# Kernel optimization log

Measured on AMD Instinct MI355X. Metric: run time of the kernel, lower is better.

Reference implementation:

```python
import jax, jax.numpy as jnp
import numpy as np

B, T, J, D = 32, 1024, 256, 512

def setup_inputs() -> dict:
    key = jax.random.key(0)
    k1, k2, k3 = jax.random.split(key, 3)
    h = jax.random.normal(k1, (B, T, D), dtype=jnp.float32)
    u = jax.random.normal(k2, (B, J, D), dtype=jnp.float32)
    w = jax.random.normal(k3, (1, 3 * D), dtype=jnp.float32) * 0.05
    return {"h": h, "u": u, "w": w}

def reference(h, u, w):
    # S[b,i,j] = w . concat([h_i, u_j, h_i*u_j])
    # Algebraic decomposition: w = [w_h, w_u, w_m]
    d = h.shape[-1]
    w = w[0]
    w_h, w_u, w_m = w[:d], w[d:2*d], w[2*d:]
    # [B,T,1] + [B,1,J] + [B,T,J]
    term_h = jnp.einsum('btd,d->bt', h, w_h)[:, :, None]
    term_u = jnp.einsum('bjd,d->bj', u, w_u)[:, None, :]
    term_m = jnp.einsum('btd,bjd->btj', h * w_m, u)
    return term_h + term_u + term_m
```

## Files before the change

### kernel.cpp

```cpp
#include <hip/hip_runtime.h>
#include <hip/hip_bf16.h>
#include <stdint.h>

#define B_ 32
#define T_ 1024
#define J_ 256
#define D_ 512

typedef __attribute__((ext_vector_type(8))) short short8;
typedef __attribute__((ext_vector_type(4))) float floatx4;

__global__ __launch_bounds__(256) void prep_u_kernel(
    const float* __restrict__ u, const float* __restrict__ w,
    __hip_bfloat16* __restrict__ B2, float* __restrict__ tu)
{
    int row  = blockIdx.x * 4 + (threadIdx.x >> 6);
    int lane = threadIdx.x & 63;
    const float* src = u + (size_t)row * D_;
    int base = lane * 8;

    float4 v0  = *(const float4*)(src + base);
    float4 v1  = *(const float4*)(src + base + 4);
    float4 wh0 = *(const float4*)(w + base);
    float4 wh1 = *(const float4*)(w + base + 4);
    float4 wu0 = *(const float4*)(w + D_ + base);
    float4 wu1 = *(const float4*)(w + D_ + base + 4);
    float4 wm0 = *(const float4*)(w + 2*D_ + base);
    float4 wm1 = *(const float4*)(w + 2*D_ + base + 4);

    float s = v0.x*wu0.x + v0.y*wu0.y + v0.z*wu0.z + v0.w*wu0.w
            + v1.x*wu1.x + v1.y*wu1.y + v1.z*wu1.z + v1.w*wu1.w;

    float vals[8] = {
        v0.x*wm0.x + wh0.x, v0.y*wm0.y + wh0.y,
        v0.z*wm0.z + wh0.z, v0.w*wm0.w + wh0.w,
        v1.x*wm1.x + wh1.x, v1.y*wm1.y + wh1.y,
        v1.z*wm1.z + wh1.z, v1.w*wm1.w + wh1.w };

    union { __hip_bfloat16 b[8]; uint4 q; } pk;
#pragma unroll
    for (int i = 0; i < 8; i++) pk.b[i] = __float2bfloat16(vals[i]);
    *(uint4*)(B2 + (size_t)row * D_ + base) = pk.q;

#pragma unroll
    for (int off = 32; off > 0; off >>= 1) s += __shfl_down(s, off, 64);
    if (lane == 0) tu[row] = s;
}

__device__ inline void gload_lds16(const void* g, void* l) {
    __builtin_amdgcn_global_load_lds(
        (__attribute__((address_space(1))) void*)(g),
        (__attribute__((address_space(3))) void*)(l),
        16, 0, 0);
}

__global__ __launch_bounds__(256) void gemm_kernel(
    const float* __restrict__ h,
    const __hip_bfloat16* __restrict__ B2,
    const float* __restrict__ tu,
    float* __restrict__ out)
{
    __shared__ __align__(16) __hip_bfloat16 sA[64 * 32];
    __shared__ __align__(16) __hip_bfloat16 sB[128 * 32];

    const int b   = blockIdx.y;
    const int tM  = blockIdx.x >> 1;
    const int tN  = blockIdx.x & 1;
    const int tid = threadIdx.x;
    const int w = tid >> 6, lane = tid & 63;
    const int wr = w >> 1, wc = w & 1;

    const float*          Ah = h  + ((size_t)b * T_ + tM * 64) * D_;
    const __hip_bfloat16* Bb = B2 + ((size_t)b * J_ + tN * 128) * D_;

    const int srow = tid >> 2;
    const int scb  = ((tid & 3) ^ ((tid >> 3) & 3));
    const int ssc  = scb * 8;
    const int ldsOff = tid * 8;

    floatx4 acc[2][4];
#pragma unroll
    for (int i = 0; i < 2; i++)
#pragma unroll
        for (int j = 0; j < 4; j++) acc[i][j] = (floatx4)0.0f;

    const int cb = lane >> 4;
    const int fr = lane & 15;

    for (int k0 = 0; k0 < D_; k0 += 32) {
        gload_lds16(Bb + (size_t)srow        * D_ + k0 + ssc, sB + ldsOff);
        gload_lds16(Bb + (size_t)(srow + 64) * D_ + k0 + ssc, sB + 64 * 32 + ldsOff);

        {
            const float* ap = Ah + (size_t)srow * D_ + k0 + ssc;
            float4 a0 = *(const float4*)(ap);
            float4 a1 = *(const float4*)(ap + 4);
            union { __hip_bfloat16 b[8]; uint4 q; } pk;
            pk.b[0]=__float2bfloat16(a0.x); pk.b[1]=__float2bfloat16(a0.y);
            pk.b[2]=__float2bfloat16(a0.z); pk.b[3]=__float2bfloat16(a0.w);
            pk.b[4]=__float2bfloat16(a1.x); pk.b[5]=__float2bfloat16(a1.y);
            pk.b[6]=__float2bfloat16(a1.z); pk.b[7]=__float2bfloat16(a1.w);
            *(uint4*)(sA + ldsOff) = pk.q;
        }
        __syncthreads();

        short8 af[2], bfr[4];
#pragma unroll
        for (int mi = 0; mi < 2; mi++) {
            int rr = wr * 32 + mi * 16 + fr;
            af[mi] = *(const short8*)(sA + rr * 32 + ((cb ^ ((rr >> 1) & 3)) << 3));
        }
#pragma unroll
        for (int ni = 0; ni < 4; ni++) {
            int rr = wc * 64 + ni * 16 + fr;
            bfr[ni] = *(const short8*)(sB + rr * 32 + ((cb ^ ((rr >> 1) & 3)) << 3));
        }
#pragma unroll
        for (int mi = 0; mi < 2; mi++)
#pragma unroll
            for (int ni = 0; ni < 4; ni++)
                acc[mi][ni] = __builtin_amdgcn_mfma_f32_16x16x32_bf16(
                    af[mi], bfr[ni], acc[mi][ni], 0, 0, 0);
        __syncthreads();
    }

    const size_t outB = (size_t)b * T_ * J_;
    const int colq = lane & 15;
    const int rq   = (lane >> 4) * 4;
    const float* tub = tu + b * J_;
#pragma unroll
    for (int mi = 0; mi < 2; mi++) {
        int r0 = tM * 64 + wr * 32 + mi * 16 + rq;
#pragma unroll
        for (int ni = 0; ni < 4; ni++) {
            int col = tN * 128 + wc * 64 + ni * 16 + colq;
            float tuv = tub[col];
#pragma unroll
            for (int r = 0; r < 4; r++) {
                out[outB + (size_t)(r0 + r) * J_ + col] =
                    acc[mi][ni][r] + tuv;
            }
        }
    }
}

extern "C" void kernel_launch(void* const* d_in, const int* in_sizes, int n_in,
                              void* d_out, int out_size, void* d_ws, size_t ws_size,
                              hipStream_t stream)
{
    const float* h = (const float*)d_in[0];
    const float* u = (const float*)d_in[1];
    const float* w = (const float*)d_in[2];
    float* out = (float*)d_out;

    uint8_t* ws = (uint8_t*)d_ws;
    __hip_bfloat16* B2 = (__hip_bfloat16*)ws;
    float* tu = (float*)(ws + (size_t)B_ * J_ * D_ * 2);

    prep_u_kernel<<<dim3(B_ * J_ / 4), 256, 0, stream>>>(u, w, B2, tu);

    gemm_kernel<<<dim3((T_ / 64) * (J_ / 128), B_), 256, 0, stream>>>(h, B2, tu, out);
}
```

Before: 139.5 us.

## Stage half-K B tiles in LDS and stream A fragments directly from global

The GEMM now uses 512-thread blocks covering 128x128 output tiles. Each block stages half of K (256 columns) of the bf16 B tile into a 64KB XOR-swizzled LDS buffer, so there are only two barrier phases instead of sixteen. Each wave loads its own 16 rows of fp32 h straight from global into registers, converts them to bf16 and runs 8 MFMAs per k-step, which removes the A staging through LDS. In exchange, B cannot be double-buffered, the large LDS footprint limits occupancy, and the uncoalesced per-lane A loads could stall the MFMAs.

```diff
diff --git a/kernel.cpp b/kernel.cpp
--- a/kernel.cpp
+++ b/kernel.cpp
@@ -54,92 +54,72 @@
         16, 0, 0);
 }
 
-__global__ __launch_bounds__(256) void gemm_kernel(
+__global__ __launch_bounds__(512, 4) void gemm_kernel(
     const float* __restrict__ h,
     const __hip_bfloat16* __restrict__ B2,
     const float* __restrict__ tu,
     float* __restrict__ out)
 {
-    __shared__ __align__(16) __hip_bfloat16 sA[64 * 32];
-    __shared__ __align__(16) __hip_bfloat16 sB[128 * 32];
+    __shared__ __align__(16) __hip_bfloat16 sB[128 * 256];
 
     const int b   = blockIdx.y;
     const int tM  = blockIdx.x >> 1;
     const int tN  = blockIdx.x & 1;
     const int tid = threadIdx.x;
     const int w = tid >> 6, lane = tid & 63;
-    const int wr = w >> 1, wc = w & 1;
 
-    const float*          Ah = h  + ((size_t)b * T_ + tM * 64) * D_;
+    const int fr = lane & 15;
+    const int kq = lane >> 4;
+
+    const float* Aw = h + ((size_t)b * T_ + tM * 128 + w * 16 + fr) * D_;
     const __hip_bfloat16* Bb = B2 + ((size_t)b * J_ + tN * 128) * D_;
 
-    const int srow = tid >> 2;
-    const int scb  = ((tid & 3) ^ ((tid >> 3) & 3));
-    const int ssc  = scb * 8;
-    const int ldsOff = tid * 8;
+    floatx4 acc[8];
+#pragma unroll
+    for (int n = 0; n < 8; n++) acc[n] = (floatx4)0.0f;
 
-    floatx4 acc[2][4];
+    for (int p = 0; p < 2; p++) {
 #pragma unroll
-    for (int i = 0; i < 2; i++)
-#pragma unroll
-        for (int j = 0; j < 4; j++) acc[i][j] = (floatx4)0.0f;
-
-    const int cb = lane >> 4;
-    const int fr = lane & 15;
-
-    for (int k0 = 0; k0 < D_; k0 += 32) {
-        gload_lds16(Bb + (size_t)srow        * D_ + k0 + ssc, sB + ldsOff);
-        gload_lds16(Bb + (size_t)(srow + 64) * D_ + k0 + ssc, sB + 64 * 32 + ldsOff);
-
-        {
-            const float* ap = Ah + (size_t)srow * D_ + k0 + ssc;
-            float4 a0 = *(const float4*)(ap);
-            float4 a1 = *(const float4*)(ap + 4);
-            union { __hip_bfloat16 b[8]; uint4 q; } pk;
-            pk.b[0]=__float2bfloat16(a0.x); pk.b[1]=__float2bfloat16(a0.y);
-            pk.b[2]=__float2bfloat16(a0.z); pk.b[3]=__float2bfloat16(a0.w);
-            pk.b[4]=__float2bfloat16(a1.x); pk.b[5]=__float2bfloat16(a1.y);
-            pk.b[6]=__float2bfloat16(a1.z); pk.b[7]=__float2bfloat16(a1.w);
-            *(uint4*)(sA + ldsOff) = pk.q;
+        for (int i = 0; i < 8; i++) {
+            int q  = i * 512 + tid;
+            int j  = q >> 5;
+            int c  = (q & 31) ^ (j & 31);
+            gload_lds16(Bb + (size_t)j * D_ + p * 256 + c * 8, sB + q * 8);
         }
         __syncthreads();
 
-        short8 af[2], bfr[4];
 #pragma unroll
-        for (int mi = 0; mi < 2; mi++) {
-            int rr = wr * 32 + mi * 16 + fr;
-            af[mi] = *(const short8*)(sA + rr * 32 + ((cb ^ ((rr >> 1) & 3)) << 3));
+        for (int ks = 0; ks < 8; ks++) {
+            const float* ap = Aw + p * 256 + ks * 32 + kq * 8;
+            float4 a0 = *(const float4*)(ap);
+            float4 a1 = *(const float4*)(ap + 4);
+            union { __hip_bfloat16 e[8]; short8 v; } af;
+            af.e[0]=__float2bfloat16(a0.x); af.e[1]=__float2bfloat16(a0.y);
+            af.e[2]=__float2bfloat16(a0.z); af.e[3]=__float2bfloat16(a0.w);
+            af.e[4]=__float2bfloat16(a1.x); af.e[5]=__float2bfloat16(a1.y);
+            af.e[6]=__float2bfloat16(a1.z); af.e[7]=__float2bfloat16(a1.w);
+#pragma unroll
+            for (int n = 0; n < 8; n++) {
+                int j = n * 16 + fr;
+                int c = ks * 4 + kq;
+                short8 bf = *(const short8*)(sB + ((j * 32) + (c ^ (j & 31))) * 8);
+                acc[n] = __builtin_amdgcn_mfma_f32_16x16x32_bf16(
+                    af.v, bf, acc[n], 0, 0, 0);
+            }
         }
-#pragma unroll
-        for (int ni = 0; ni < 4; ni++) {
-            int rr = wc * 64 + ni * 16 + fr;
-            bfr[ni] = *(const short8*)(sB + rr * 32 + ((cb ^ ((rr >> 1) & 3)) << 3));
-        }
-#pragma unroll
-        for (int mi = 0; mi < 2; mi++)
-#pragma unroll
-            for (int ni = 0; ni < 4; ni++)
-                acc[mi][ni] = __builtin_amdgcn_mfma_f32_16x16x32_bf16(
-                    af[mi], bfr[ni], acc[mi][ni], 0, 0, 0);
         __syncthreads();
     }
 
     const size_t outB = (size_t)b * T_ * J_;
-    const int colq = lane & 15;
-    const int rq   = (lane >> 4) * 4;
+    const int r0 = tM * 128 + w * 16 + (lane >> 4) * 4;
     const float* tub = tu + b * J_;
 #pragma unroll
-    for (int mi = 0; mi < 2; mi++) {
-        int r0 = tM * 64 + wr * 32 + mi * 16 + rq;
+    for (int n = 0; n < 8; n++) {
+        int col = tN * 128 + n * 16 + fr;
+        float tuv = tub[col];
 #pragma unroll
-        for (int ni = 0; ni < 4; ni++) {
-            int col = tN * 128 + wc * 64 + ni * 16 + colq;
-            float tuv = tub[col];
-#pragma unroll
-            for (int r = 0; r < 4; r++) {
-                out[outB + (size_t)(r0 + r) * J_ + col] =
-                    acc[mi][ni][r] + tuv;
-            }
+        for (int r = 0; r < 4; r++) {
+            out[outB + (size_t)(r0 + r) * J_ + col] = acc[n][r] + tuv;
         }
     }
 }
@@ -159,5 +139,5 @@
 
     prep_u_kernel<<<dim3(B_ * J_ / 4), 256, 0, stream>>>(u, w, B2, tu);
 
-    gemm_kernel<<<dim3((T_ / 64) * (J_ / 128), B_), 256, 0, stream>>>(h, B2, tu, out);
+    gemm_kernel<<<dim3((T_ / 128) * (J_ / 128), B_), 512, 0, stream>>>(h, B2, tu, out);
 }
```

After: 131.7 us. 1.06x faster.

## Double-buffer GEMM tiles with async LDS loads and convert A from fp32 in LDS

Applied to the files above, without the earlier changes.

The GEMM main loop becomes a two-stage double buffer. The next k-slice is fetched with global_load_lds while the current one is computed, which cuts the sync stalls per iteration from two to one. The A operand (h) now goes to LDS as fp32 through async loads with an XOR swizzle, and is converted to bf16 when fragments are read, instead of being loaded through registers and converted before the LDS store. The B layout drops its swizzle and launch bounds ask for 4 blocks per CU. In exchange, LDS use per block rises and each fragment read now does the conversion.

```diff
diff --git a/kernel.cpp b/kernel.cpp
--- a/kernel.cpp
+++ b/kernel.cpp
@@ -54,14 +54,14 @@
         16, 0, 0);
 }
 
-__global__ __launch_bounds__(256) void gemm_kernel(
+__global__ __launch_bounds__(256, 4) void gemm_kernel(
     const float* __restrict__ h,
     const __hip_bfloat16* __restrict__ B2,
     const float* __restrict__ tu,
     float* __restrict__ out)
 {
-    __shared__ __align__(16) __hip_bfloat16 sA[64 * 32];
-    __shared__ __align__(16) __hip_bfloat16 sB[128 * 32];
+    __shared__ __align__(16) float          sA[2][64 * 32];
+    __shared__ __align__(16) __hip_bfloat16 sB[2][128 * 32];
 
     const int b   = blockIdx.y;
     const int tM  = blockIdx.x >> 1;
@@ -69,14 +69,23 @@
     const int tid = threadIdx.x;
     const int w = tid >> 6, lane = tid & 63;
     const int wr = w >> 1, wc = w & 1;
+    const int fr = lane & 15;
+    const int kq = lane >> 4;
 
-    const float*          Ah = h  + ((size_t)b * T_ + tM * 64) * D_;
+    const float*          Ab = h  + ((size_t)b * T_ + tM * 64) * D_;
     const __hip_bfloat16* Bb = B2 + ((size_t)b * J_ + tN * 128) * D_;
 
-    const int srow = tid >> 2;
-    const int scb  = ((tid & 3) ^ ((tid >> 3) & 3));
-    const int ssc  = scb * 8;
-    const int ldsOff = tid * 8;
+    int ajr[2], acs[2];
+#pragma unroll
+    for (int i = 0; i < 2; i++) {
+        int q = i * 256 + tid;
+        ajr[i] = q >> 3;
+        acs[i] = (q & 7) ^ (ajr[i] & 7);
+    }
+    int bjr[2];
+#pragma unroll
+    for (int i = 0; i < 2; i++) bjr[i] = (i * 256 + tid) >> 2;
+    const int bcs = tid & 3;
 
     floatx4 acc[2][4];
 #pragma unroll
@@ -84,36 +93,53 @@
 #pragma unroll
         for (int j = 0; j < 4; j++) acc[i][j] = (floatx4)0.0f;
 
-    const int cb = lane >> 4;
-    const int fr = lane & 15;
+#pragma unroll
+    for (int i = 0; i < 2; i++)
+        gload_lds16(Ab + (size_t)ajr[i] * D_ + acs[i] * 4,
+                    &sA[0][(i * 256 + tid) * 4]);
+#pragma unroll
+    for (int i = 0; i < 2; i++)
+        gload_lds16(Bb + (size_t)bjr[i] * D_ + bcs * 8,
+                    &sB[0][(i * 256 + tid) * 8]);
+    __syncthreads();
 
-    for (int k0 = 0; k0 < D_; k0 += 32) {
-        gload_lds16(Bb + (size_t)srow        * D_ + k0 + ssc, sB + ldsOff);
-        gload_lds16(Bb + (size_t)(srow + 64) * D_ + k0 + ssc, sB + 64 * 32 + ldsOff);
+    for (int p = 0; p < 16; p++) {
+        if (p < 15) {
+            int k0 = (p + 1) * 32;
+            int nb = (p + 1) & 1;
+#pragma unroll
+            for (int i = 0; i < 2; i++)
+                gload_lds16(Ab + (size_t)ajr[i] * D_ + k0 + acs[i] * 4,
+                            &sA[nb][(i * 256 + tid) * 4]);
+#pragma unroll
+            for (int i = 0; i < 2; i++)
+                gload_lds16(Bb + (size_t)bjr[i] * D_ + k0 + bcs * 8,
+                            &sB[nb][(i * 256 + tid) * 8]);
+        }
 
-        {
-            const float* ap = Ah + (size_t)srow * D_ + k0 + ssc;
-            float4 a0 = *(const float4*)(ap);
-            float4 a1 = *(const float4*)(ap + 4);
-            union { __hip_bfloat16 b[8]; uint4 q; } pk;
-            pk.b[0]=__float2bfloat16(a0.x); pk.b[1]=__float2bfloat16(a0.y);
-            pk.b[2]=__float2bfloat16(a0.z); pk.b[3]=__float2bfloat16(a0.w);
-            pk.b[4]=__float2bfloat16(a1.x); pk.b[5]=__float2bfloat16(a1.y);
-            pk.b[6]=__float2bfloat16(a1.z); pk.b[7]=__float2bfloat16(a1.w);
-            *(uint4*)(sA + ldsOff) = pk.q;
+        const float*          sAp = sA[p & 1];
+        const __hip_bfloat16* sBp = sB[p & 1];
+
+        short8 bfr[4];
+#pragma unroll
+        for (int ni = 0; ni < 4; ni++) {
+            int jb = wc * 64 + ni * 16 + fr;
+            bfr[ni] = *(const short8*)(sBp + (jb * 4 + kq) * 8);
         }
-        __syncthreads();
-
-        short8 af[2], bfr[4];
+        short8 af[2];
 #pragma unroll
         for (int mi = 0; mi < 2; mi++) {
-            int rr = wr * 32 + mi * 16 + fr;
-            af[mi] = *(const short8*)(sA + rr * 32 + ((cb ^ ((rr >> 1) & 3)) << 3));
-        }
-#pragma unroll
-        for (int ni = 0; ni < 4; ni++) {
-            int rr = wc * 64 + ni * 16 + fr;
-            bfr[ni] = *(const short8*)(sB + rr * 32 + ((cb ^ ((rr >> 1) & 3)) << 3));
+            int ja = wr * 32 + mi * 16 + fr;
+            int s0 = (2 * kq)     ^ (ja & 7);
+            int s1 = (2 * kq + 1) ^ (ja & 7);
+            float4 x0 = *(const float4*)(sAp + (ja * 8 + s0) * 4);
+            float4 x1 = *(const float4*)(sAp + (ja * 8 + s1) * 4);
+            union { __hip_bfloat16 e[8]; short8 v; } pk;
+            pk.e[0]=__float2bfloat16(x0.x); pk.e[1]=__float2bfloat16(x0.y);
+            pk.e[2]=__float2bfloat16(x0.z); pk.e[3]=__float2bfloat16(x0.w);
+            pk.e[4]=__float2bfloat16(x1.x); pk.e[5]=__float2bfloat16(x1.y);
+            pk.e[6]=__float2bfloat16(x1.z); pk.e[7]=__float2bfloat16(x1.w);
+            af[mi] = pk.v;
         }
 #pragma unroll
         for (int mi = 0; mi < 2; mi++)
@@ -121,24 +147,22 @@
             for (int ni = 0; ni < 4; ni++)
                 acc[mi][ni] = __builtin_amdgcn_mfma_f32_16x16x32_bf16(
                     af[mi], bfr[ni], acc[mi][ni], 0, 0, 0);
+
         __syncthreads();
     }
 
     const size_t outB = (size_t)b * T_ * J_;
-    const int colq = lane & 15;
-    const int rq   = (lane >> 4) * 4;
     const float* tub = tu + b * J_;
 #pragma unroll
     for (int mi = 0; mi < 2; mi++) {
-        int r0 = tM * 64 + wr * 32 + mi * 16 + rq;
+        int r0 = tM * 64 + wr * 32 + mi * 16 + kq * 4;
 #pragma unroll
         for (int ni = 0; ni < 4; ni++) {
-            int col = tN * 128 + wc * 64 + ni * 16 + colq;
+            int col = tN * 128 + wc * 64 + ni * 16 + fr;
             float tuv = tub[col];
 #pragma unroll
             for (int r = 0; r < 4; r++) {
-                out[outB + (size_t)(r0 + r) * J_ + col] =
-                    acc[mi][ni][r] + tuv;
+                out[outB + (size_t)(r0 + r) * J_ + col] = acc[mi][ni][r] + tuv;
             }
         }
     }
```

Result: no change. 140.4 us (+0.6%).
